# Performance work log

Measured on AMD Instinct MI355X. Metric: run time of the kernel, lower is better.

Reference implementation:

```python
import jax, jax.numpy as jnp
import numpy as np

B, N, DIM, H, DH = 2, 2048, 1024, 16, 64
INNER = H * DH


def _rotate_half(t):
    # interleaved pairs: (..., d) -> rotate each (x1, x2) pair to (-x2, x1)
    t = t.reshape(*t.shape[:-1], -1, 2)
    x1, x2 = t[..., 0], t[..., 1]
    return jnp.stack((-x2, x1), axis=-1).reshape(*t.shape[:-2], -1)


def _apply_rotary(freqs, t):
    # freqs: [B, N, DH] -> broadcast over heads; t: [B, H, N, DH]
    f = freqs[:, None, :, :]
    return t * jnp.cos(f) + _rotate_half(t) * jnp.sin(f)


def _layernorm(x, g, b, eps=1e-5):
    mu = jnp.mean(x, axis=-1, keepdims=True)
    var = jnp.mean((x - mu) ** 2, axis=-1, keepdims=True)
    return (x - mu) * jax.lax.rsqrt(var + eps) * g + b


def setup_inputs() -> dict:
    key = jax.random.key(0)
    ks = jax.random.split(key, 8)
    x = jax.random.normal(ks[0], (B, N, DIM), jnp.float32)
    rotary = jax.random.normal(ks[1], (B, N, DH), jnp.float32)
    ln_g = jnp.ones((DIM,), jnp.float32)
    ln_b = jnp.zeros((DIM,), jnp.float32)
    w_qkv = jax.random.normal(ks[2], (DIM, 3 * INNER), jnp.float32) / np.sqrt(DIM)
    b_qkv = jnp.zeros((3 * INNER,), jnp.float32)
    w_out = jax.random.normal(ks[3], (INNER, DIM), jnp.float32) / np.sqrt(INNER)
    b_out = jnp.zeros((DIM,), jnp.float32)
    return {"x": x, "rotary": rotary, "ln_g": ln_g, "ln_b": ln_b,
            "w_qkv": w_qkv, "b_qkv": b_qkv, "w_out": w_out, "b_out": b_out}


def reference(x, rotary, ln_g, ln_b, w_qkv, b_qkv, w_out, b_out):
    h = _layernorm(x, ln_g, ln_b)
    qkv = h @ w_qkv + b_qkv                      # [B, N, 3*INNER]
    q, k, v = jnp.split(qkv, 3, axis=-1)
    # b n (h d) -> b h n d
    def to_heads(t):
        return t.reshape(B, N, H, DH).transpose(0, 2, 1, 3)
    q, k, v = to_heads(q), to_heads(k), to_heads(v)
    q = _apply_rotary(rotary, q)
    k = _apply_rotary(rotary, k)
    v = _apply_rotary(rotary, v)                 # rotate_value=True
    scale = DH ** (-0.5)
    attn = jnp.einsum('bhnd,bhmd->bhnm', q, k) * scale
    attn = jax.nn.softmax(attn, axis=-1)
    out = jnp.einsum('bhnm,bhmd->bhnd', attn, v)
    out = _apply_rotary(-rotary, out)            # inverse rotation on values
    out = out.transpose(0, 2, 1, 3).reshape(B, N, INNER)
    return out @ w_out + b_out
```

## Files before the change

kernel.cpp:

```cpp
#include <hip/hip_runtime.h>
#include <hip/hip_bf16.h>

typedef _Float16 f16;
typedef __attribute__((ext_vector_type(4))) float f32x4;
typedef __attribute__((ext_vector_type(8))) _Float16 f16x8;
typedef __attribute__((ext_vector_type(4))) _Float16 f16x4;
typedef __attribute__((ext_vector_type(2))) __fp16 hf2;

#define Bv 2
#define Nv 2048
#define DIMv 1024
#define Hv 16
#define DHv 64
#define INNERv 1024
#define QKV3v 3072

__device__ __forceinline__ void gload16(const void* g, void* l) {
  __builtin_amdgcn_global_load_lds(
      (const __attribute__((address_space(1))) void*)g,
      (__attribute__((address_space(3))) void*)l, 16, 0, 0);
}

__global__ __launch_bounds__(256) void ln_kernel(
    const float* __restrict__ x, const float* __restrict__ g,
    const float* __restrict__ bb, f16* __restrict__ h) {
  const int row = blockIdx.x;
  const int t = threadIdx.x;
  const float4 v = reinterpret_cast<const float4*>(x + (size_t)row * DIMv)[t];
  float s = v.x + v.y + v.z + v.w;
  float sq = v.x * v.x + v.y * v.y + v.z * v.z + v.w * v.w;
#pragma unroll
  for (int o = 32; o > 0; o >>= 1) {
    s += __shfl_down(s, o);
    sq += __shfl_down(sq, o);
  }
  __shared__ float red[8];
  __shared__ float musr[2];
  const int wave = t >> 6, lane = t & 63;
  if (lane == 0) { red[wave] = s; red[4 + wave] = sq; }
  __syncthreads();
  if (t == 0) {
    const float S = red[0] + red[1] + red[2] + red[3];
    const float SQ = red[4] + red[5] + red[6] + red[7];
    const float mu = S * (1.0f / DIMv);
    const float var = SQ * (1.0f / DIMv) - mu * mu;
    musr[0] = mu;
    musr[1] = rsqrtf(var + 1e-5f);
  }
  __syncthreads();
  const float mu = musr[0], rs = musr[1];
  const float4 gv = reinterpret_cast<const float4*>(g)[t];
  const float4 bv = reinterpret_cast<const float4*>(bb)[t];
  f16x4 o;
  o.x = (f16)((v.x - mu) * rs * gv.x + bv.x);
  o.y = (f16)((v.y - mu) * rs * gv.y + bv.y);
  o.z = (f16)((v.z - mu) * rs * gv.z + bv.z);
  o.w = (f16)((v.w - mu) * rs * gv.w + bv.w);
  *reinterpret_cast<f16x4*>(&h[(size_t)row * DIMv + t * 4]) = o;
}

__global__ __launch_bounds__(256) void rotcs_kernel(
    const float* __restrict__ rot, float* __restrict__ c,
    float* __restrict__ s, int n) {
  const int i = blockIdx.x * blockDim.x + threadIdx.x;
  if (i < n) {
    const float f = rot[i];
    c[i] = cosf(f);
    s[i] = sinf(f);
  }
}

__global__ __launch_bounds__(256) void transpose_f16(
    const float* __restrict__ W, f16* __restrict__ Wt, int K, int N) {
  __shared__ float tile[64][65];
  const int t = threadIdx.x;
  const int n0 = blockIdx.x * 64, k0 = blockIdx.y * 64;
#pragma unroll
  for (int i = 0; i < 16; ++i) {
    const int idx = t + i * 256;
    const int r = idx >> 6, c = idx & 63;
    tile[r][c] = W[(size_t)(k0 + r) * N + n0 + c];
  }
  __syncthreads();
#pragma unroll
  for (int i = 0; i < 16; ++i) {
    const int idx = t + i * 256;
    const int r = idx >> 6, c = idx & 63;
    Wt[(size_t)(n0 + r) * K + k0 + c] = (f16)tile[c][r];
  }
}

template <int EPI>
__global__ __launch_bounds__(256) void gemm_mfma(
    const f16* __restrict__ A, const f16* __restrict__ Bt,
    const float* __restrict__ bias, void* __restrict__ Cout,
    const float* __restrict__ cs, const float* __restrict__ sn,
    int M, int N, int K) {
  __shared__ __align__(16) f16 Asb[2][128 * 32];
  __shared__ __align__(16) f16 Bsb[2][128 * 32];
  const int t = threadIdx.x;
  const int l = t & 63, w = t >> 6;
  const int wr = w >> 1, wc = w & 1;

  const int nwg = gridDim.x;
  const int wg = blockIdx.x;
  const int nid = (wg & 7) * (nwg >> 3) + (wg >> 3);
  const int rows = M >> 7;
  const int by = nid % rows;
  const int bx = nid / rows;
  const int row0 = by * 128, col0 = bx * 128;

  const int i1 = t, i2 = t + 256;
  const f16* ga1 = &A[(size_t)(row0 + (i1 >> 2)) * K + (i1 & 3) * 8];
  const f16* ga2 = &A[(size_t)(row0 + (i2 >> 2)) * K + (i2 & 3) * 8];
  const f16* gb1 = &Bt[(size_t)(col0 + (i1 >> 2)) * K + (i1 & 3) * 8];
  const f16* gb2 = &Bt[(size_t)(col0 + (i2 >> 2)) * K + (i2 & 3) * 8];
  const int a_off1 = w * 512, a_off2 = w * 512 + 2048;

  const int rl = l & 15, kg = l >> 4;
  const int ar = (wr * 64 + rl) * 32 + kg * 8;
  const int br = (wc * 64 + rl) * 32 + kg * 8;

  const f32x4 zero = {0.f, 0.f, 0.f, 0.f};
  f32x4 acc[4][4];
#pragma unroll
  for (int m = 0; m < 4; ++m)
#pragma unroll
    for (int n = 0; n < 4; ++n) acc[m][n] = zero;

#define GSTAGE(buf, kk)                           \
  {                                               \
    gload16(ga1 + (kk)*32, &Asb[buf][a_off1]);    \
    gload16(ga2 + (kk)*32, &Asb[buf][a_off2]);    \
    gload16(gb1 + (kk)*32, &Bsb[buf][a_off1]);    \
    gload16(gb2 + (kk)*32, &Bsb[buf][a_off2]);    \
  }

  const int nt = K >> 5;
  GSTAGE(0, 0);

  for (int kt = 0; kt < nt; ++kt) {
    const int cur = kt & 1;
    if (kt + 1 < nt) {
      GSTAGE(cur ^ 1, kt + 1);
      asm volatile("s_waitcnt vmcnt(4)" ::: "memory");
    } else {
      asm volatile("s_waitcnt vmcnt(0)" ::: "memory");
    }
    __builtin_amdgcn_s_barrier();
    __builtin_amdgcn_sched_barrier(0);
    f16x8 af[4], bf[4];
#pragma unroll
    for (int m = 0; m < 4; ++m)
      af[m] = *reinterpret_cast<const f16x8*>(&Asb[cur][ar + m * 16 * 32]);
#pragma unroll
    for (int n = 0; n < 4; ++n)
      bf[n] = *reinterpret_cast<const f16x8*>(&Bsb[cur][br + n * 16 * 32]);
#pragma unroll
    for (int m = 0; m < 4; ++m)
#pragma unroll
      for (int n = 0; n < 4; ++n)
        acc[m][n] =
            __builtin_amdgcn_mfma_f32_16x16x32_f16(af[m], bf[n], acc[m][n], 0, 0, 0);
    asm volatile("" ::: "memory");
    __builtin_amdgcn_s_barrier();
    __builtin_amdgcn_sched_barrier(0);
  }
#undef GSTAGE

#pragma unroll
  for (int m = 0; m < 4; ++m) {
#pragma unroll
    for (int n = 0; n < 4; ++n) {
#pragma unroll
      for (int jr = 0; jr < 4; ++jr) {
        const int rg = row0 + wr * 64 + m * 16 + kg * 4 + jr;
        const int cg = col0 + wc * 64 + n * 16 + rl;
        const float v = acc[m][n][jr] + bias[cg];
        if (EPI == 0) {
          ((float*)Cout)[(size_t)rg * N + cg] = v;
        } else {
          const float p = __shfl_xor(v, 1);
          const size_t cb = (size_t)rg * DHv + (cg & 63);
          const float cc = cs[cb], ss = sn[cb];
          const float y = (l & 1) ? (v * cc + p * ss) : (v * cc - p * ss);
          ((f16*)Cout)[(size_t)rg * N + cg] = (f16)y;
        }
      }
    }
  }
}

__global__ __launch_bounds__(256) void prep_kv(
    const f16* __restrict__ qkvf, f16* __restrict__ Kimg,
    f16* __restrict__ Vimg) {
  const int nt = blockIdx.x, hh = blockIdx.y, b = blockIdx.z;
  const int t = threadIdx.x;
  const size_t tbase = ((size_t)((b * Hv + hh) * 32 + nt)) << 12;

#pragma unroll
  for (int half = 0; half < 2; ++half) {
    const int task = t + half * 256;
    const int key = task >> 3, c = task & 7;
    const int d = (c * 8) ^ ((key & 7) << 3);
    const f16x8 kv = *reinterpret_cast<const f16x8*>(
        &qkvf[(size_t)(b * Nv + nt * 64 + key) * QKV3v + INNERv + hh * DHv + d]);
    *reinterpret_cast<f16x8*>(&Kimg[tbase + key * 64 + c * 8]) = kv;
  }

  __shared__ __align__(16) f16 tile[64][80];
  const int nl = t >> 3, dc = (t & 7) * 8;
#pragma unroll
  for (int half = 0; half < 2; ++half) {
    const int n = nl + half * 32;
    *reinterpret_cast<f16x8*>(&tile[n][dc]) = *reinterpret_cast<const f16x8*>(
        &qkvf[(size_t)(b * Nv + nt * 64 + n) * QKV3v + 2 * INNERv + hh * DHv + dc]);
  }
  __syncthreads();
  const int c0 = (t & 7) * 8;
  const int kwp = c0 >> 5, kgp = (c0 >> 3) & 3;
#pragma unroll
  for (int half = 0; half < 2; ++half) {
    const int d = (t >> 3) + half * 32;
    union { f16 e[8]; f16x8 v; } uo;
#pragma unroll
    for (int j = 0; j < 8; ++j) {
      const int mk = (j >> 2) & 1, jr = j & 3;
      const int kap = kwp * 32 + mk * 16 + kgp * 4 + jr;
      uo.e[j] = tile[kap][d];
    }
    *reinterpret_cast<f16x8*>(
        &Vimg[tbase + d * 64 + (c0 ^ ((d & 7) << 3))]) = uo.v;
  }
}

__global__ __launch_bounds__(256, 4) void attn_mfma(
    const f16* __restrict__ qkvf, const f16* __restrict__ Kimg,
    const f16* __restrict__ Vimg, const float* __restrict__ cs,
    const float* __restrict__ sn, f16* __restrict__ ao) {
  const int wg = blockIdx.x;
  const int swz = (wg & 7) * 128 + (wg >> 3);
  const int qb = swz & 31;
  const int hh = (swz >> 5) & 15;
  const int b = swz >> 9;
  const int t = threadIdx.x, l = t & 63, w = t >> 6;
  const int qw = w >> 1, kw = w & 1;
  const int rl = l & 15, kg = l >> 4;

  __shared__ __align__(16) f16 KsB[2][4096];
  __shared__ __align__(16) f16 VtB[2][4096];
  __shared__ float Lbuf[2][2][32];

  const size_t qrow0 = (size_t)(b * Nv + qb * 64 + qw * 32);
  f16x8 bq[2][2];
#pragma unroll
  for (int nq = 0; nq < 2; ++nq)
#pragma unroll
    for (int ks = 0; ks < 2; ++ks)
      bq[nq][ks] = *reinterpret_cast<const f16x8*>(
          &qkvf[(qrow0 + nq * 16 + rl) * QKV3v + hh * DHv + ks * 32 + kg * 8]);

  f16x8 ones;
#pragma unroll
  for (int j = 0; j < 8; ++j) ones[j] = (f16)1.0f;

  const f32x4 zero = {0.f, 0.f, 0.f, 0.f};
  f32x4 o_acc[2][4];
  f32x4 l_acc[2] = {zero, zero};
#pragma unroll
  for (int nq = 0; nq < 2; ++nq)
#pragma unroll
    for (int m2 = 0; m2 < 4; ++m2) o_acc[nq][m2] = zero;

  const size_t ibase = (((size_t)((b * Hv + hh) * 32)) << 12) + w * 512 + l * 8;
  const f16* kimg_t = Kimg + ibase;
  const f16* vimg_t = Vimg + ibase;

#define STAGEI(buf, tile)                                          \
  {                                                                \
    gload16(kimg_t + ((tile) << 12), &KsB[buf][w * 512]);          \
    gload16(kimg_t + ((tile) << 12) + 2048, &KsB[buf][w * 512 + 2048]); \
    gload16(vimg_t + ((tile) << 12), &VtB[buf][w * 512]);          \
    gload16(vimg_t + ((tile) << 12) + 2048, &VtB[buf][w * 512 + 2048]); \
  }

  STAGEI(0, 0);

  const float SC2 = 0.125f * 1.44269504f;

  for (int kt = 0; kt < 32; ++kt) {
    const int cur = kt & 1;
    if (kt + 1 < 32) {
      STAGEI(cur ^ 1, kt + 1);
      asm volatile("s_waitcnt vmcnt(4)" ::: "memory");
    } else {
      asm volatile("s_waitcnt vmcnt(0)" ::: "memory");
    }
    __builtin_amdgcn_s_barrier();
    __builtin_amdgcn_sched_barrier(0);

    const f16* Kc = &KsB[cur][0];
    const f16* Vc = &VtB[cur][0];

    f16x8 ak[2][2];
#pragma unroll
    for (int mk = 0; mk < 2; ++mk)
#pragma unroll
      for (int ks = 0; ks < 2; ++ks)
        ak[mk][ks] = *reinterpret_cast<const f16x8*>(
            &Kc[((kw * 32 + mk * 16 + rl) << 6) |
                ((ks * 32 + kg * 8) ^ ((rl & 7) << 3))]);
    f16x8 av[4];
#pragma unroll
    for (int m2 = 0; m2 < 4; ++m2)
      av[m2] = *reinterpret_cast<const f16x8*>(
          &Vc[((m2 * 16 + rl) << 6) |
              ((kw * 32 + kg * 8) ^ ((rl & 7) << 3))]);

    f32x4 sa[2][2];
#pragma unroll
    for (int mk = 0; mk < 2; ++mk)
#pragma unroll
      for (int nq = 0; nq < 2; ++nq) sa[mk][nq] = zero;
    __builtin_amdgcn_s_setprio(1);
#pragma unroll
    for (int ks = 0; ks < 2; ++ks)
#pragma unroll
      for (int mk = 0; mk < 2; ++mk)
#pragma unroll
        for (int nq = 0; nq < 2; ++nq)
          sa[mk][nq] = __builtin_amdgcn_mfma_f32_16x16x32_f16(
              ak[mk][ks], bq[nq][ks], sa[mk][nq], 0, 0, 0);
    __builtin_amdgcn_s_setprio(0);

    f16x8 pb[2];
#pragma unroll
    for (int nq = 0; nq < 2; ++nq) {
      float p00 = exp2f(fminf(sa[0][nq][0] * SC2, 13.0f));
      float p01 = exp2f(fminf(sa[0][nq][1] * SC2, 13.0f));
      float p02 = exp2f(fminf(sa[0][nq][2] * SC2, 13.0f));
      float p03 = exp2f(fminf(sa[0][nq][3] * SC2, 13.0f));
      float p10 = exp2f(fminf(sa[1][nq][0] * SC2, 13.0f));
      float p11 = exp2f(fminf(sa[1][nq][1] * SC2, 13.0f));
      float p12 = exp2f(fminf(sa[1][nq][2] * SC2, 13.0f));
      float p13 = exp2f(fminf(sa[1][nq][3] * SC2, 13.0f));
      union { hf2 h2[4]; f16x8 v; } u;
      u.h2[0] = __builtin_amdgcn_cvt_pkrtz(p00, p01);
      u.h2[1] = __builtin_amdgcn_cvt_pkrtz(p02, p03);
      u.h2[2] = __builtin_amdgcn_cvt_pkrtz(p10, p11);
      u.h2[3] = __builtin_amdgcn_cvt_pkrtz(p12, p13);
      pb[nq] = u.v;
    }

    __builtin_amdgcn_s_setprio(1);
#pragma unroll
    for (int nq = 0; nq < 2; ++nq)
      l_acc[nq] = __builtin_amdgcn_mfma_f32_16x16x32_f16(
          ones, pb[nq], l_acc[nq], 0, 0, 0);
#pragma unroll
    for (int nq = 0; nq < 2; ++nq)
#pragma unroll
      for (int m2 = 0; m2 < 4; ++m2)
        o_acc[nq][m2] = __builtin_amdgcn_mfma_f32_16x16x32_f16(
            av[m2], pb[nq], o_acc[nq][m2], 0, 0, 0);
    __builtin_amdgcn_s_setprio(0);

    asm volatile("" ::: "memory");
    __builtin_amdgcn_s_barrier();
    __builtin_amdgcn_sched_barrier(0);
  }
#undef STAGEI

  if (kg == 0) {
    Lbuf[qw][kw][rl] = l_acc[0][0];
    Lbuf[qw][kw][16 + rl] = l_acc[1][0];
  }
  {
    char* ob = (qw == 0 ? (char*)KsB : (char*)VtB) + kw * 8192;
#pragma unroll
    for (int nq = 0; nq < 2; ++nq)
#pragma unroll
      for (int m2 = 0; m2 < 4; ++m2)
        *reinterpret_cast<f32x4*>(
            ob + (nq * 16 + rl) * 256 +
            ((m2 * 64 + kg * 16) ^ ((rl & 7) << 4))) = o_acc[nq][m2];
  }
  __syncthreads();
  {
    const int q_local = w * 16 + (l >> 2);
    const int qw_r = q_local >> 5, q_in = q_local & 31;
    const int d0 = (l & 3) * 16;
    char* rb = (qw_r == 0 ? (char*)KsB : (char*)VtB);
    const float linv = 1.0f / (Lbuf[qw_r][0][q_in] + Lbuf[qw_r][1][q_in]);
    const size_t nq_g = (size_t)(b * Nv + qb * 64 + q_local);
    const size_t cb = nq_g * DHv + d0;
    union { f16 e[16]; f16x8 v[2]; } uo;
#pragma unroll
    for (int j = 0; j < 4; ++j) {
      const unsigned off = q_in * 256 + (((l & 3) * 64 + j * 16) ^ ((q_in & 7) << 4));
      const f32x4 a = *reinterpret_cast<const f32x4*>(rb + off);
      const f32x4 c2 = *reinterpret_cast<const f32x4*>(rb + 8192 + off);
      const float4 csv = *reinterpret_cast<const float4*>(&cs[cb + j * 4]);
      const float4 snv = *reinterpret_cast<const float4*>(&sn[cb + j * 4]);
      const float o0 = (a[0] + c2[0]) * linv;
      const float o1 = (a[1] + c2[1]) * linv;
      const float o2 = (a[2] + c2[2]) * linv;
      const float o3 = (a[3] + c2[3]) * linv;
      uo.e[j * 4 + 0] = (f16)(o0 * csv.x + o1 * snv.x);
      uo.e[j * 4 + 1] = (f16)(o1 * csv.y - o0 * snv.y);
      uo.e[j * 4 + 2] = (f16)(o2 * csv.z + o3 * snv.z);
      uo.e[j * 4 + 3] = (f16)(o3 * csv.w - o2 * snv.w);
    }
    f16* aop = &ao[nq_g * INNERv + hh * DHv + d0];
    *reinterpret_cast<f16x8*>(aop) = uo.v[0];
    *reinterpret_cast<f16x8*>(aop + 8) = uo.v[1];
  }
}

extern "C" void kernel_launch(void* const* d_in, const int* in_sizes, int n_in,
                              void* d_out, int out_size, void* d_ws, size_t ws_size,
                              hipStream_t stream) {
  (void)in_sizes; (void)n_in; (void)out_size; (void)ws_size;
  const float* x = (const float*)d_in[0];
  const float* rot = (const float*)d_in[1];
  const float* ln_g = (const float*)d_in[2];
  const float* ln_b = (const float*)d_in[3];
  const float* w_qkv = (const float*)d_in[4];
  const float* b_qkv = (const float*)d_in[5];
  const float* w_out = (const float*)d_in[6];
  const float* b_out = (const float*)d_in[7];

  char* p = (char*)d_ws;
  f16* h = (f16*)p;            p += (size_t)Bv * Nv * DIMv * 2;
  float* cs = (float*)p;       p += (size_t)Bv * Nv * DHv * 4;
  float* sn = (float*)p;       p += (size_t)Bv * Nv * DHv * 4;
  f16* wqT = (f16*)p;          p += (size_t)QKV3v * DIMv * 2;
  f16* woT = (f16*)p;          p += (size_t)DIMv * INNERv * 2;
  f16* qkvf = (f16*)p;         p += (size_t)Bv * Nv * QKV3v * 2;
  f16* ao = (f16*)p;           p += (size_t)Bv * Nv * INNERv * 2;
  f16* Kimg = (f16*)p;         p += (size_t)Bv * Hv * 32 * 4096 * 2;
  f16* Vimg = (f16*)p;         p += (size_t)Bv * Hv * 32 * 4096 * 2;

  ln_kernel<<<dim3(Bv * Nv), dim3(256), 0, stream>>>(x, ln_g, ln_b, h);
  rotcs_kernel<<<dim3((Bv * Nv * DHv) / 256), dim3(256), 0, stream>>>(
      rot, cs, sn, Bv * Nv * DHv);
  transpose_f16<<<dim3(QKV3v / 64, DIMv / 64), dim3(256), 0, stream>>>(
      w_qkv, wqT, DIMv, QKV3v);
  transpose_f16<<<dim3(INNERv / 64, DIMv / 64), dim3(256), 0, stream>>>(
      w_out, woT, DIMv, INNERv);
  gemm_mfma<1><<<dim3((QKV3v / 128) * ((Bv * Nv) / 128)), dim3(256), 0, stream>>>(
      h, wqT, b_qkv, (void*)qkvf, cs, sn, Bv * Nv, QKV3v, DIMv);
  prep_kv<<<dim3(Nv / 64, Hv, Bv), dim3(256), 0, stream>>>(qkvf, Kimg, Vimg);
  attn_mfma<<<dim3(1024), dim3(256), 0, stream>>>(qkvf, Kimg, Vimg, cs, sn, ao);
  gemm_mfma<0><<<dim3((DIMv / 128) * ((Bv * Nv) / 128)), dim3(256), 0, stream>>>(
      ao, woT, b_out, d_out, nullptr, nullptr, Bv * Nv, DIMv, INNERv);
}
```

Measured before the change: 163.9 us.

## Double attention query tile per block to 128 rows and drop GEMM swizzle

The attention kernel now runs 512 threads (8 waves) per block, each block covering 128 queries instead of 64. The K/V tile staged in LDS is shared by twice as many query rows, halving K/V global loads per query, and the per-wave staging drops from four to two loads. The two key-split partial outputs are now combined in LDS with an extra barrier pass. The GEMM's XCD-aware block-index swizzle is replaced by a plain 2D grid, which may hurt L2 locality across chiplets.

```diff
diff --git a/kernel.cpp b/kernel.cpp
--- a/kernel.cpp
+++ b/kernel.cpp
@@ -101,14 +101,7 @@
   const int t = threadIdx.x;
   const int l = t & 63, w = t >> 6;
   const int wr = w >> 1, wc = w & 1;
-
-  const int nwg = gridDim.x;
-  const int wg = blockIdx.x;
-  const int nid = (wg & 7) * (nwg >> 3) + (wg >> 3);
-  const int rows = M >> 7;
-  const int by = nid % rows;
-  const int bx = nid / rows;
-  const int row0 = by * 128, col0 = bx * 128;
+  const int row0 = blockIdx.y * 128, col0 = blockIdx.x * 128;
 
   const int i1 = t, i2 = t + 256;
   const f16* ga1 = &A[(size_t)(row0 + (i1 >> 2)) * K + (i1 & 3) * 8];
@@ -234,24 +227,24 @@
   }
 }
 
-__global__ __launch_bounds__(256, 4) void attn_mfma(
+__global__ __launch_bounds__(512, 4) void attn_mfma(
     const f16* __restrict__ qkvf, const f16* __restrict__ Kimg,
     const f16* __restrict__ Vimg, const float* __restrict__ cs,
     const float* __restrict__ sn, f16* __restrict__ ao) {
   const int wg = blockIdx.x;
-  const int swz = (wg & 7) * 128 + (wg >> 3);
-  const int qb = swz & 31;
-  const int hh = (swz >> 5) & 15;
-  const int b = swz >> 9;
+  const int swz = (wg & 7) * 64 + (wg >> 3);
+  const int qb = swz & 15;
+  const int hh = (swz >> 4) & 15;
+  const int b = swz >> 8;
   const int t = threadIdx.x, l = t & 63, w = t >> 6;
   const int qw = w >> 1, kw = w & 1;
   const int rl = l & 15, kg = l >> 4;
 
   __shared__ __align__(16) f16 KsB[2][4096];
   __shared__ __align__(16) f16 VtB[2][4096];
-  __shared__ float Lbuf[2][2][32];
-
-  const size_t qrow0 = (size_t)(b * Nv + qb * 64 + qw * 32);
+  __shared__ float Lbuf[4][2][32];
+
+  const size_t qrow0 = (size_t)(b * Nv + qb * 128 + qw * 32);
   f16x8 bq[2][2];
 #pragma unroll
   for (int nq = 0; nq < 2; ++nq)
@@ -276,12 +269,10 @@
   const f16* kimg_t = Kimg + ibase;
   const f16* vimg_t = Vimg + ibase;
 
-#define STAGEI(buf, tile)                                          \
-  {                                                                \
-    gload16(kimg_t + ((tile) << 12), &KsB[buf][w * 512]);          \
-    gload16(kimg_t + ((tile) << 12) + 2048, &KsB[buf][w * 512 + 2048]); \
-    gload16(vimg_t + ((tile) << 12), &VtB[buf][w * 512]);          \
-    gload16(vimg_t + ((tile) << 12) + 2048, &VtB[buf][w * 512 + 2048]); \
+#define STAGEI(buf, tile)                                   \
+  {                                                         \
+    gload16(kimg_t + ((size_t)(tile) << 12), &KsB[buf][w * 512]); \
+    gload16(vimg_t + ((size_t)(tile) << 12), &VtB[buf][w * 512]); \
   }
 
   STAGEI(0, 0);
@@ -292,7 +283,7 @@
     const int cur = kt & 1;
     if (kt + 1 < 32) {
       STAGEI(cur ^ 1, kt + 1);
-      asm volatile("s_waitcnt vmcnt(4)" ::: "memory");
+      asm volatile("s_waitcnt vmcnt(2)" ::: "memory");
     } else {
       asm volatile("s_waitcnt vmcnt(0)" ::: "memory");
     }
@@ -375,8 +366,8 @@
     Lbuf[qw][kw][rl] = l_acc[0][0];
     Lbuf[qw][kw][16 + rl] = l_acc[1][0];
   }
-  {
-    char* ob = (qw == 0 ? (char*)KsB : (char*)VtB) + kw * 8192;
+  char* ob = (qw < 2 ? (char*)KsB : (char*)VtB) + (qw & 1) * 8192;
+  if (kw == 1) {
 #pragma unroll
     for (int nq = 0; nq < 2; ++nq)
 #pragma unroll
@@ -386,26 +377,37 @@
             ((m2 * 64 + kg * 16) ^ ((rl & 7) << 4))) = o_acc[nq][m2];
   }
   __syncthreads();
+  if (kw == 0) {
+#pragma unroll
+    for (int nq = 0; nq < 2; ++nq)
+#pragma unroll
+      for (int m2 = 0; m2 < 4; ++m2) {
+        f32x4* slot = reinterpret_cast<f32x4*>(
+            ob + (nq * 16 + rl) * 256 +
+            ((m2 * 64 + kg * 16) ^ ((rl & 7) << 4)));
+        *slot = *slot + o_acc[nq][m2];
+      }
+  }
+  __syncthreads();
   {
     const int q_local = w * 16 + (l >> 2);
     const int qw_r = q_local >> 5, q_in = q_local & 31;
     const int d0 = (l & 3) * 16;
-    char* rb = (qw_r == 0 ? (char*)KsB : (char*)VtB);
+    char* rb = (qw_r < 2 ? (char*)KsB : (char*)VtB) + (qw_r & 1) * 8192;
     const float linv = 1.0f / (Lbuf[qw_r][0][q_in] + Lbuf[qw_r][1][q_in]);
-    const size_t nq_g = (size_t)(b * Nv + qb * 64 + q_local);
+    const size_t nq_g = (size_t)(b * Nv + qb * 128 + q_local);
     const size_t cb = nq_g * DHv + d0;
     union { f16 e[16]; f16x8 v[2]; } uo;
 #pragma unroll
     for (int j = 0; j < 4; ++j) {
       const unsigned off = q_in * 256 + (((l & 3) * 64 + j * 16) ^ ((q_in & 7) << 4));
       const f32x4 a = *reinterpret_cast<const f32x4*>(rb + off);
-      const f32x4 c2 = *reinterpret_cast<const f32x4*>(rb + 8192 + off);
       const float4 csv = *reinterpret_cast<const float4*>(&cs[cb + j * 4]);
       const float4 snv = *reinterpret_cast<const float4*>(&sn[cb + j * 4]);
-      const float o0 = (a[0] + c2[0]) * linv;
-      const float o1 = (a[1] + c2[1]) * linv;
-      const float o2 = (a[2] + c2[2]) * linv;
-      const float o3 = (a[3] + c2[3]) * linv;
+      const float o0 = a[0] * linv;
+      const float o1 = a[1] * linv;
+      const float o2 = a[2] * linv;
+      const float o3 = a[3] * linv;
       uo.e[j * 4 + 0] = (f16)(o0 * csv.x + o1 * snv.x);
       uo.e[j * 4 + 1] = (f16)(o1 * csv.y - o0 * snv.y);
       uo.e[j * 4 + 2] = (f16)(o2 * csv.z + o3 * snv.z);
@@ -448,10 +450,10 @@
       w_qkv, wqT, DIMv, QKV3v);
   transpose_f16<<<dim3(INNERv / 64, DIMv / 64), dim3(256), 0, stream>>>(
       w_out, woT, DIMv, INNERv);
-  gemm_mfma<1><<<dim3((QKV3v / 128) * ((Bv * Nv) / 128)), dim3(256), 0, stream>>>(
+  gemm_mfma<1><<<dim3(QKV3v / 128, (Bv * Nv) / 128), dim3(256), 0, stream>>>(
       h, wqT, b_qkv, (void*)qkvf, cs, sn, Bv * Nv, QKV3v, DIMv);
   prep_kv<<<dim3(Nv / 64, Hv, Bv), dim3(256), 0, stream>>>(qkvf, Kimg, Vimg);
-  attn_mfma<<<dim3(1024), dim3(256), 0, stream>>>(qkvf, Kimg, Vimg, cs, sn, ao);
-  gemm_mfma<0><<<dim3((DIMv / 128) * ((Bv * Nv) / 128)), dim3(256), 0, stream>>>(
+  attn_mfma<<<dim3(512), dim3(512), 0, stream>>>(qkvf, Kimg, Vimg, cs, sn, ao);
+  gemm_mfma<0><<<dim3(DIMv / 128, (Bv * Nv) / 128), dim3(256), 0, stream>>>(
       ao, woT, b_out, d_out, nullptr, nullptr, Bv * Nv, DIMv, INNERv);
 }
```

Result: no change. 160.8 us (-1.9%).
